# Performance work log

Hardware: AMD Instinct MI355X
Metric: run time of the kernel (lower is better)

## Reference

```python
import jax, jax.numpy as jnp
import numpy as np

N_NODES = 50000
N_EDGES = 800000
D_IN, D_HID, D_LAT = 128, 128, 64
BN_EPS = 1e-5


def setup_inputs() -> dict:
    key = jax.random.key(0)
    ks = jax.random.split(key, 8)
    x = jax.random.normal(ks[0], (N_NODES, D_IN), dtype=jnp.float32)
    edge_index = jax.random.randint(ks[1], (2, N_EDGES), 0, N_NODES, dtype=jnp.int64)
    s1 = 1.0 / np.sqrt(D_IN)
    s2 = 1.0 / np.sqrt(D_HID)
    W1 = jax.random.normal(ks[2], (D_IN, D_HID), dtype=jnp.float32) * s1
    b1 = jnp.zeros((D_HID,), jnp.float32)
    gamma = jnp.ones((D_HID,), jnp.float32)
    beta = jnp.zeros((D_HID,), jnp.float32)
    Wmu = jax.random.normal(ks[3], (D_HID, D_LAT), dtype=jnp.float32) * s2
    bmu = jnp.zeros((D_LAT,), jnp.float32)
    Wls = jax.random.normal(ks[4], (D_HID, D_LAT), dtype=jnp.float32) * s2
    bls = jnp.zeros((D_LAT,), jnp.float32)
    return {"x": x, "edge_index": edge_index, "W1": W1, "b1": b1,
            "gamma": gamma, "beta": beta, "Wmu": Wmu, "bmu": bmu,
            "Wls": Wls, "bls": bls}


def _gcn_conv(h, src, dst, norm_e, inv_deg, W, b):
    # PyG GCNConv: linear transform, then sym-normalized aggregation (A+I).
    h = h @ W                                   # [N, F]
    msgs = h[src] * norm_e[:, None]             # gather + edge scaling, [E, F]
    agg = jax.ops.segment_sum(msgs, dst, num_segments=h.shape[0])
    # self-loop contribution: norm[i]*norm[i] = 1/deg[i]
    return agg + h * inv_deg[:, None] + b


def reference(x, edge_index, W1, b1, gamma, beta, Wmu, bmu, Wls, bls):
    src, dst = edge_index[0], edge_index[1]
    n = x.shape[0]
    # degrees including self loops (GCN symmetric normalization)
    deg = jax.ops.segment_sum(jnp.ones(dst.shape, x.dtype), dst, num_segments=n) + 1.0
    inv_sqrt_deg = jax.lax.rsqrt(deg)
    norm_e = inv_sqrt_deg[src] * inv_sqrt_deg[dst]   # per-edge norm, [E]
    inv_deg = 1.0 / deg

    h = _gcn_conv(x, src, dst, norm_e, inv_deg, W1, b1)
    # BatchNorm1d with batch statistics (biased var), then ReLU; dropout off (eval)
    mean = h.mean(axis=0)
    var = h.var(axis=0)
    h = (h - mean) * jax.lax.rsqrt(var + BN_EPS) * gamma + beta
    h = jax.nn.relu(h)

    mu = _gcn_conv(h, src, dst, norm_e, inv_deg, Wmu, bmu)
    log_std = _gcn_conv(h, src, dst, norm_e, inv_deg, Wls, bls)
    return mu, log_std
```

## Files before the change

kernel.cpp:

```cpp
#include <hip/hip_runtime.h>
#include <hip/hip_bf16.h>

#define N_NODES 50000
#define N_EDGES 800000
#define F 128
#define L 64
#define BN_EPS 1e-5f
#define SCAN_BLOCKS 196
#define BN_BLOCKS 391
#define NPART 8
#define PART_SZ 6250
#define FILL_BLOCKS 2048

typedef __attribute__((ext_vector_type(8))) short short8;
typedef __attribute__((ext_vector_type(8))) unsigned short ushort8;
typedef __attribute__((ext_vector_type(4))) float f32x4;

static __device__ __forceinline__ float loadF(const void* p, int i, int f32) {
    if (f32) return ((const float*)p)[i];
    return __bfloat162float(((const __hip_bfloat16*)p)[i]);
}
static __device__ __forceinline__ int loadI(const void* p, int i, int i64) {
    if (i64) return (int)((const long long*)p)[i];
    return ((const int*)p)[i];
}
static __device__ __forceinline__ float bfu2f(unsigned short u) {
    unsigned int t = ((unsigned int)u) << 16;
    float f;
    __builtin_memcpy(&f, &t, 4);
    return f;
}
static __device__ __forceinline__ short f2bf_s(float f) {
    union { __hip_bfloat16 b; short s; } cv;
    cv.b = __float2bfloat16(f);
    return cv.s;
}
static __device__ __forceinline__ unsigned short f2bf_u(float f) {
    union { __hip_bfloat16 b; unsigned short u; } cv;
    cv.b = __float2bfloat16(f);
    return cv.u;
}

__global__ void k_prep(const void* __restrict__ W1, const void* __restrict__ Wmu,
                       const void* __restrict__ Wls, const unsigned short* __restrict__ xs,
                       const int* __restrict__ ei, __hip_bfloat16* __restrict__ Wt1,
                       __hip_bfloat16* __restrict__ Wt2, int* __restrict__ flags,
                       int* __restrict__ degi) {
    int b = blockIdx.x;
    int t = threadIdx.x;
    if (b == 0) {
        __shared__ int cnt[2];
        if (t < 2) cnt[t] = 0;
        __syncthreads();
        unsigned short v = xs[2 * t];
        int e = (v >> 7) & 0xff;
        int sane = (e >= 112 && e <= 133) ? 1 : 0;
        if (v == 0 || v == 0x8000) sane = 1;
        atomicAdd(&cnt[0], sane);
        atomicAdd(&cnt[1], (ei[2 * t + 1] != 0) ? 1 : 0);
        __syncthreads();
        if (t == 0) {
            flags[0] = (cnt[0] < 128) ? 1 : 0;
            flags[1] = (cnt[1] < 8) ? 1 : 0;
        }
    } else if (b <= 64) {
        __shared__ int cnt;
        if (t == 0) cnt = 0;
        __syncthreads();
        unsigned short v = ((const unsigned short*)W1)[2 * t];
        int e = (v >> 7) & 0xff;
        atomicAdd(&cnt, (e >= 100 && e <= 133) ? 1 : 0);
        __syncthreads();
        int f32 = (cnt < 128) ? 1 : 0;
        int idx = (b - 1) * 256 + t;
        int n = idx >> 7, k = idx & 127;
        Wt1[idx] = __float2bfloat16(loadF(W1, k * F + n, f32));
        float v2 = (n < L) ? loadF(Wmu, k * L + n, f32) : loadF(Wls, k * L + (n - L), f32);
        Wt2[idx] = __float2bfloat16(v2);
    } else {
        int i = (b - 65) * 256 + t;
        if (i < N_NODES) degi[i] = 0;
    }
}

__global__ void k_eiprep(const void* ei, const int* __restrict__ flags,
                         int* __restrict__ src32, int* __restrict__ dst32,
                         int* __restrict__ degi) {
    int e = blockIdx.x * blockDim.x + threadIdx.x;
    if (e < N_EDGES) {
        int i64 = flags[1];
        int d = loadI(ei, N_EDGES + e, i64);
        if (i64) {
            src32[e] = loadI(ei, e, 1);
            dst32[e] = d;
        }
        atomicAdd(&degi[d], 1);
    }
}

__global__ void k_bsum(const int* __restrict__ degi, int* __restrict__ bsum) {
    int i = blockIdx.x * 256 + threadIdx.x;
    int v = (i < N_NODES) ? degi[i] : 0;
#pragma unroll
    for (int o = 32; o; o >>= 1) v += __shfl_down(v, o);
    __shared__ int ws[4];
    if ((threadIdx.x & 63) == 0) ws[threadIdx.x >> 6] = v;
    __syncthreads();
    if (threadIdx.x == 0) bsum[blockIdx.x] = ws[0] + ws[1] + ws[2] + ws[3];
}

__global__ void k_scanb(const int* __restrict__ bsum, int* __restrict__ boff,
                        int* __restrict__ offs) {
    __shared__ int s[256];
    int t = threadIdx.x;
    int v = (t < SCAN_BLOCKS) ? bsum[t] : 0;
    s[t] = v;
    __syncthreads();
    for (int o = 1; o < 256; o <<= 1) {
        int u = (t >= o) ? s[t - o] : 0;
        __syncthreads();
        s[t] += u;
        __syncthreads();
    }
    boff[t] = s[t] - v;
    if (t == 0) offs[N_NODES] = N_EDGES;
}

__global__ void k_offs(int* __restrict__ degi, const int* __restrict__ boff,
                       int* __restrict__ offs, float* __restrict__ isd) {
    __shared__ int s[256];
    int i = blockIdx.x * 256 + threadIdx.x;
    int t = threadIdx.x;
    int v = (i < N_NODES) ? degi[i] : 0;
    s[t] = v;
    __syncthreads();
    for (int o = 1; o < 256; o <<= 1) {
        int u = (t >= o) ? s[t - o] : 0;
        __syncthreads();
        s[t] += u;
        __syncthreads();
    }
    if (i < N_NODES) {
        offs[i] = boff[blockIdx.x] + s[t] - v;
        isd[i] = 1.0f / sqrtf((float)v + 1.0f);
        degi[i] = 0;
    }
}

__global__ void k_fill(const int* __restrict__ ei32, const int* __restrict__ src32,
                       const int* __restrict__ dst32, const int* __restrict__ flags,
                       const int* __restrict__ offs, int* __restrict__ cur,
                       int* __restrict__ csr) {
    const int* sp;
    const int* dp;
    if (flags[1]) { sp = src32; dp = dst32; }
    else          { sp = ei32;  dp = ei32 + N_EDGES; }
    int grp = blockIdx.x & (NPART - 1);
    int sub = blockIdx.x >> 3;
    int lo = grp * PART_SZ, hi = lo + PART_SZ;
    int stride = (FILL_BLOCKS >> 3) * 256;
    for (int e = sub * 256 + threadIdx.x; e < N_EDGES; e += stride) {
        int d = dp[e];
        if (d >= lo && d < hi) {
            int pos = offs[d] + atomicAdd(&cur[d], 1);
            csr[pos] = sp[e];
        }
    }
}

__global__ __launch_bounds__(256) void k_gemm_mfma(const void* __restrict__ Xin,
        const __hip_bfloat16* __restrict__ Wt, const float* __restrict__ isd,
        const int* __restrict__ flags, int mode,
        const float* __restrict__ bnscale, const float* __restrict__ bnshift,
        unsigned short* __restrict__ outb) {
    int wave = threadIdx.x >> 6, lane = threadIdx.x & 63;
    int quad = lane >> 4, mr = lane & 15;
    int m0 = blockIdx.x * 64 + wave * 16;
    int row = m0 + mr;
    if (row >= N_NODES) row = N_NODES - 1;
    short8 a[4];
    if (mode == 1) {
        const unsigned short* xb = (const unsigned short*)Xin;
#pragma unroll
        for (int t = 0; t < 4; ++t) {
            int k0 = t * 32 + quad * 8;
            ushort8 raw = *(const ushort8*)(xb + row * F + k0);
            short8 av;
#pragma unroll
            for (int j = 0; j < 8; ++j) {
                float v = bfu2f(raw[j]) * bnscale[k0 + j] + bnshift[k0 + j];
                av[j] = f2bf_s(fmaxf(v, 0.f));
            }
            a[t] = av;
        }
    } else if (flags[0]) {
        const float* xf = (const float*)Xin;
#pragma unroll
        for (int t = 0; t < 4; ++t) {
            int off = row * F + t * 32 + quad * 8;
            short8 av;
#pragma unroll
            for (int j = 0; j < 8; ++j) av[j] = f2bf_s(xf[off + j]);
            a[t] = av;
        }
    } else {
        const short* xb = (const short*)Xin;
#pragma unroll
        for (int t = 0; t < 4; ++t)
            a[t] = *(const short8*)(xb + row * F + t * 32 + quad * 8);
    }
    f32x4 acc[8];
    const short* wb = (const short*)Wt;
#pragma unroll
    for (int nt = 0; nt < 8; ++nt) {
        const short* wp = wb + (nt * 16 + mr) * F + quad * 8;
        f32x4 c = {0.f, 0.f, 0.f, 0.f};
        c = __builtin_amdgcn_mfma_f32_16x16x32_bf16(a[0], *(const short8*)(wp), c, 0, 0, 0);
        c = __builtin_amdgcn_mfma_f32_16x16x32_bf16(a[1], *(const short8*)(wp + 32), c, 0, 0, 0);
        c = __builtin_amdgcn_mfma_f32_16x16x32_bf16(a[2], *(const short8*)(wp + 64), c, 0, 0, 0);
        c = __builtin_amdgcn_mfma_f32_16x16x32_bf16(a[3], *(const short8*)(wp + 96), c, 0, 0, 0);
        acc[nt] = c;
    }
    float sd[4];
    int orow[4];
#pragma unroll
    for (int r = 0; r < 4; ++r) {
        orow[r] = m0 + quad * 4 + r;
        sd[r] = (orow[r] < N_NODES) ? isd[orow[r]] : 0.f;
    }
#pragma unroll
    for (int nt = 0; nt < 8; ++nt)
#pragma unroll
        for (int r = 0; r < 4; ++r)
            if (orow[r] < N_NODES)
                outb[orow[r] * F + nt * 16 + mr] = f2bf_u(acc[nt][r] * sd[r]);
}

__global__ void k_agg1(const unsigned short* __restrict__ val, const int* __restrict__ csr,
                       const int* __restrict__ offs, const float* __restrict__ isd,
                       const void* __restrict__ b1, const int* __restrict__ flags,
                       unsigned short* __restrict__ out) {
    int node = blockIdx.x * 4 + (threadIdx.x >> 6);
    if (node >= N_NODES) return;
    int lane = threadIdx.x & 63;
    int grp = lane >> 4, l16 = lane & 15;
    const ushort8* vp = (const ushort8*)val;
    float acc[8] = {0.f, 0.f, 0.f, 0.f, 0.f, 0.f, 0.f, 0.f};
    if (grp == 0) {
        ushort8 u = vp[node * 16 + l16];
#pragma unroll
        for (int j = 0; j < 8; ++j) acc[j] = bfu2f(u[j]);
    }
    int end = offs[node + 1];
    int i = offs[node] + grp;
    for (; i + 4 < end; i += 8) {
        ushort8 u0 = vp[csr[i] * 16 + l16];
        ushort8 u1 = vp[csr[i + 4] * 16 + l16];
#pragma unroll
        for (int j = 0; j < 8; ++j) acc[j] += bfu2f(u0[j]) + bfu2f(u1[j]);
    }
    for (; i < end; i += 4) {
        ushort8 u = vp[csr[i] * 16 + l16];
#pragma unroll
        for (int j = 0; j < 8; ++j) acc[j] += bfu2f(u[j]);
    }
#pragma unroll
    for (int j = 0; j < 8; ++j) {
        acc[j] += __shfl_xor(acc[j], 16);
        acc[j] += __shfl_xor(acc[j], 32);
    }
    if (grp == 0) {
        float sd = isd[node];
        int c0 = l16 * 8, f32 = flags[0];
        ushort8 r;
#pragma unroll
        for (int j = 0; j < 8; ++j) r[j] = f2bf_u(acc[j] * sd + loadF(b1, c0 + j, f32));
        ((ushort8*)out)[node * 16 + l16] = r;
    }
}

__global__ void k_bnstats(const unsigned short* __restrict__ h, float* __restrict__ partial) {
    __shared__ float ls[256][8];
    __shared__ float lq[256][8];
    int t = threadIdx.x;
    int o = t & 15, rg = t >> 4;
    int row0 = blockIdx.x * 128 + rg;
    float s[8] = {0.f}, q[8] = {0.f};
#pragma unroll
    for (int i = 0; i < 8; ++i) {
        int row = row0 + i * 16;
        if (row < N_NODES) {
            ushort8 u = *(const ushort8*)(h + row * F + o * 8);
#pragma unroll
            for (int j = 0; j < 8; ++j) {
                float v = bfu2f(u[j]);
                s[j] += v;
                q[j] += v * v;
            }
        }
    }
#pragma unroll
    for (int j = 0; j < 8; ++j) { ls[t][j] = s[j]; lq[t][j] = q[j]; }
    __syncthreads();
    if (t < 128) {
        int c = t, oo = c >> 3, jj = c & 7;
        float ts = 0.f, tq = 0.f;
#pragma unroll
        for (int rgi = 0; rgi < 16; ++rgi) {
            ts += ls[rgi * 16 + oo][jj];
            tq += lq[rgi * 16 + oo][jj];
        }
        partial[blockIdx.x * 256 + c] = ts;
        partial[blockIdx.x * 256 + 128 + c] = tq;
    }
}

__global__ void k_bnredprep(const float* __restrict__ partial, const void* __restrict__ gamma,
                            const void* __restrict__ beta, const int* __restrict__ flags,
                            float* __restrict__ scale, float* __restrict__ shift) {
    int c = blockIdx.x;
    float s = 0.f, q = 0.f;
    for (int b = threadIdx.x; b < BN_BLOCKS; b += 256) {
        s += partial[b * 256 + c];
        q += partial[b * 256 + 128 + c];
    }
#pragma unroll
    for (int o = 32; o; o >>= 1) {
        s += __shfl_down(s, o);
        q += __shfl_down(q, o);
    }
    __shared__ float ws[4], wq[4];
    if ((threadIdx.x & 63) == 0) {
        ws[threadIdx.x >> 6] = s;
        wq[threadIdx.x >> 6] = q;
    }
    __syncthreads();
    if (threadIdx.x == 0) {
        float S = ws[0] + ws[1] + ws[2] + ws[3];
        float Q = wq[0] + wq[1] + wq[2] + wq[3];
        const float invN = 1.0f / (float)N_NODES;
        float m = S * invN;
        float var = Q * invN - m * m;
        int f32 = flags[0];
        float sc = loadF(gamma, c, f32) * rsqrtf(var + BN_EPS);
        scale[c] = sc;
        shift[c] = loadF(beta, c, f32) - m * sc;
    }
}

__global__ void k_agg2(const unsigned short* __restrict__ val, const int* __restrict__ csr,
                       const int* __restrict__ offs, const float* __restrict__ isd,
                       const void* __restrict__ bmu, const void* __restrict__ bls,
                       const int* __restrict__ flags, void* __restrict__ out) {
    int node = blockIdx.x * 4 + (threadIdx.x >> 6);
    if (node >= N_NODES) return;
    int lane = threadIdx.x & 63;
    int grp = lane >> 4, l16 = lane & 15;
    const ushort8* vp = (const ushort8*)val;
    float acc[8] = {0.f, 0.f, 0.f, 0.f, 0.f, 0.f, 0.f, 0.f};
    if (grp == 0) {
        ushort8 u = vp[node * 16 + l16];
#pragma unroll
        for (int j = 0; j < 8; ++j) acc[j] = bfu2f(u[j]);
    }
    int end = offs[node + 1];
    int i = offs[node] + grp;
    for (; i + 4 < end; i += 8) {
        ushort8 u0 = vp[csr[i] * 16 + l16];
        ushort8 u1 = vp[csr[i + 4] * 16 + l16];
#pragma unroll
        for (int j = 0; j < 8; ++j) acc[j] += bfu2f(u0[j]) + bfu2f(u1[j]);
    }
    for (; i < end; i += 4) {
        ushort8 u = vp[csr[i] * 16 + l16];
#pragma unroll
        for (int j = 0; j < 8; ++j) acc[j] += bfu2f(u[j]);
    }
#pragma unroll
    for (int j = 0; j < 8; ++j) {
        acc[j] += __shfl_xor(acc[j], 16);
        acc[j] += __shfl_xor(acc[j], 32);
    }
    if (grp == 0) {
        float sd = isd[node];
        int c0 = l16 * 8, f32 = flags[0];
        int hsel = (c0 >= L) ? 1 : 0;
        int cc = c0 - hsel * L;
        const void* bp = hsel ? bls : bmu;
        float o8[8];
#pragma unroll
        for (int j = 0; j < 8; ++j) o8[j] = acc[j] * sd + loadF(bp, cc + j, f32);
        long base_o = (long)hsel * (N_NODES * 64) + (long)node * 64 + cc;
        if (f32) {
            float4 r0 = make_float4(o8[0], o8[1], o8[2], o8[3]);
            float4 r1 = make_float4(o8[4], o8[5], o8[6], o8[7]);
            *(float4*)((float*)out + base_o) = r0;
            *(float4*)((float*)out + base_o + 4) = r1;
        } else {
            ushort8 r;
#pragma unroll
            for (int j = 0; j < 8; ++j) r[j] = f2bf_u(o8[j]);
            *(ushort8*)((__hip_bfloat16*)out + base_o) = r;
        }
    }
}

extern "C" void kernel_launch(void* const* d_in, const int* in_sizes, int n_in,
                              void* d_out, int out_size, void* d_ws, size_t ws_size,
                              hipStream_t stream) {
    const void* x     = d_in[0];
    const void* ei    = d_in[1];
    const void* W1    = d_in[2];
    const void* b1    = d_in[3];
    const void* gamma = d_in[4];
    const void* beta  = d_in[5];
    const void* Wmu   = d_in[6];
    const void* bmu   = d_in[7];
    const void* Wls   = d_in[8];
    const void* bls   = d_in[9];

    int*   degi  = (int*)d_ws;
    int*   offs  = degi + 50048;
    float* isd   = (float*)(offs + 50048);
    float* stats = isd + 50000;
    int*   flags = (int*)(stats + 512);
    int*   bsum  = flags + 16;
    int*   boff  = bsum + 256;
    int*   csr   = boff + 256;
    int*   src32 = csr + 800000;
    int*   dst32 = src32 + 800000;
    __hip_bfloat16* Wt1 = (__hip_bfloat16*)(dst32 + 800000);
    __hip_bfloat16* Wt2 = Wt1 + 16384;
    unsigned short* Abf = (unsigned short*)(Wt2 + 16384);
    unsigned short* Hpre = Abf + N_NODES * F;
    float* partial = (float*)(Hpre + N_NODES * F);

    const int NT = 256;
    const int AGG_BLOCKS = (N_NODES + 3) / 4;
    const int GEMM_BLOCKS = (N_NODES + 63) / 64;

    k_prep<<<65 + SCAN_BLOCKS, NT, 0, stream>>>(W1, Wmu, Wls, (const unsigned short*)x,
                                                (const int*)ei, Wt1, Wt2, flags, degi);
    k_eiprep<<<(N_EDGES + NT - 1) / NT, NT, 0, stream>>>(ei, flags, src32, dst32, degi);
    k_bsum<<<SCAN_BLOCKS, NT, 0, stream>>>(degi, bsum);
    k_scanb<<<1, NT, 0, stream>>>(bsum, boff, offs);
    k_offs<<<SCAN_BLOCKS, NT, 0, stream>>>(degi, boff, offs, isd);
    k_fill<<<FILL_BLOCKS, NT, 0, stream>>>((const int*)ei, src32, dst32, flags,
                                           offs, degi, csr);

    k_gemm_mfma<<<GEMM_BLOCKS, NT, 0, stream>>>(x, Wt1, isd, flags, 0, nullptr, nullptr, Abf);
    k_agg1<<<AGG_BLOCKS, NT, 0, stream>>>(Abf, csr, offs, isd, b1, flags, Hpre);

    k_bnstats<<<BN_BLOCKS, NT, 0, stream>>>(Hpre, partial);
    k_bnredprep<<<128, NT, 0, stream>>>(partial, gamma, beta, flags, stats, stats + 128);

    k_gemm_mfma<<<GEMM_BLOCKS, NT, 0, stream>>>(Hpre, Wt2, isd, flags, 1,
                                                stats, stats + 128, Abf);
    k_agg2<<<AGG_BLOCKS, NT, 0, stream>>>(Abf, csr, offs, isd, bmu, bls, flags, d_out);
}
```

Baseline: 315.0 us.

## Merge scan kernels into atomic-allocated offsets and co-launch CSR fill with first GEMM

Replaces the three-kernel degree scan (block sums, single-block scan, offset write) with one kernel that scans locally and reserves its base offset through an atomic counter. This means CSR segments are no longer in node order, so aggregation now reads degree plus offset instead of offs[node+1]. The CSR fill and the first feature GEMM are fused into a single launch using disjoint block ranges, so the fill's atomic-bound work can overlap the MFMA work. The GEMM also gets vectorized input and BN-parameter loads, swapped MFMA operands so each lane stores contiguous 4-element rows, and the aggregation loop is unrolled to four gathers per iteration.

```diff
diff --git a/kernel.cpp b/kernel.cpp
--- a/kernel.cpp
+++ b/kernel.cpp
@@ -11,9 +11,11 @@
 #define NPART 8
 #define PART_SZ 6250
 #define FILL_BLOCKS 2048
+#define GEMM_BLOCKS 782
 
 typedef __attribute__((ext_vector_type(8))) short short8;
 typedef __attribute__((ext_vector_type(8))) unsigned short ushort8;
+typedef __attribute__((ext_vector_type(4))) unsigned short ushortx4;
 typedef __attribute__((ext_vector_type(4))) float f32x4;
 
 static __device__ __forceinline__ float loadF(const void* p, int i, int f32) {
@@ -62,6 +64,7 @@
         if (t == 0) {
             flags[0] = (cnt[0] < 128) ? 1 : 0;
             flags[1] = (cnt[1] < 8) ? 1 : 0;
+            flags[2] = 0;
         }
     } else if (b <= 64) {
         __shared__ int cnt;
@@ -98,39 +101,13 @@
     }
 }
 
-__global__ void k_bsum(const int* __restrict__ degi, int* __restrict__ bsum) {
-    int i = blockIdx.x * 256 + threadIdx.x;
-    int v = (i < N_NODES) ? degi[i] : 0;
-#pragma unroll
-    for (int o = 32; o; o >>= 1) v += __shfl_down(v, o);
-    __shared__ int ws[4];
-    if ((threadIdx.x & 63) == 0) ws[threadIdx.x >> 6] = v;
-    __syncthreads();
-    if (threadIdx.x == 0) bsum[blockIdx.x] = ws[0] + ws[1] + ws[2] + ws[3];
-}
-
-__global__ void k_scanb(const int* __restrict__ bsum, int* __restrict__ boff,
-                        int* __restrict__ offs) {
+__global__ void k_offs_alloc(const int* __restrict__ degi, int* __restrict__ flags,
+                             int* __restrict__ offs, float* __restrict__ isd,
+                             int* __restrict__ cur) {
     __shared__ int s[256];
+    __shared__ int base;
     int t = threadIdx.x;
-    int v = (t < SCAN_BLOCKS) ? bsum[t] : 0;
-    s[t] = v;
-    __syncthreads();
-    for (int o = 1; o < 256; o <<= 1) {
-        int u = (t >= o) ? s[t - o] : 0;
-        __syncthreads();
-        s[t] += u;
-        __syncthreads();
-    }
-    boff[t] = s[t] - v;
-    if (t == 0) offs[N_NODES] = N_EDGES;
-}
-
-__global__ void k_offs(int* __restrict__ degi, const int* __restrict__ boff,
-                       int* __restrict__ offs, float* __restrict__ isd) {
-    __shared__ int s[256];
-    int i = blockIdx.x * 256 + threadIdx.x;
-    int t = threadIdx.x;
+    int i = blockIdx.x * 256 + t;
     int v = (i < N_NODES) ? degi[i] : 0;
     s[t] = v;
     __syncthreads();
@@ -140,44 +117,25 @@
         s[t] += u;
         __syncthreads();
     }
+    if (t == 255) base = atomicAdd(&flags[2], s[255]);
+    __syncthreads();
     if (i < N_NODES) {
-        offs[i] = boff[blockIdx.x] + s[t] - v;
+        offs[i] = base + s[t] - v;
         isd[i] = 1.0f / sqrtf((float)v + 1.0f);
-        degi[i] = 0;
-    }
-}
-
-__global__ void k_fill(const int* __restrict__ ei32, const int* __restrict__ src32,
-                       const int* __restrict__ dst32, const int* __restrict__ flags,
-                       const int* __restrict__ offs, int* __restrict__ cur,
-                       int* __restrict__ csr) {
-    const int* sp;
-    const int* dp;
-    if (flags[1]) { sp = src32; dp = dst32; }
-    else          { sp = ei32;  dp = ei32 + N_EDGES; }
-    int grp = blockIdx.x & (NPART - 1);
-    int sub = blockIdx.x >> 3;
-    int lo = grp * PART_SZ, hi = lo + PART_SZ;
-    int stride = (FILL_BLOCKS >> 3) * 256;
-    for (int e = sub * 256 + threadIdx.x; e < N_EDGES; e += stride) {
-        int d = dp[e];
-        if (d >= lo && d < hi) {
-            int pos = offs[d] + atomicAdd(&cur[d], 1);
-            csr[pos] = sp[e];
-        }
-    }
-}
-
-__global__ __launch_bounds__(256) void k_gemm_mfma(const void* __restrict__ Xin,
+        cur[i] = 0;
+    }
+}
+
+static __device__ __forceinline__ void gemm_body(int bid, const void* __restrict__ Xin,
         const __hip_bfloat16* __restrict__ Wt, const float* __restrict__ isd,
         const int* __restrict__ flags, int mode,
         const float* __restrict__ bnscale, const float* __restrict__ bnshift,
         unsigned short* __restrict__ outb) {
     int wave = threadIdx.x >> 6, lane = threadIdx.x & 63;
     int quad = lane >> 4, mr = lane & 15;
-    int m0 = blockIdx.x * 64 + wave * 16;
-    int row = m0 + mr;
-    if (row >= N_NODES) row = N_NODES - 1;
+    int m0 = bid * 64 + wave * 16;
+    int node = m0 + mr;
+    int row = (node < N_NODES) ? node : N_NODES - 1;
     short8 a[4];
     if (mode == 1) {
         const unsigned short* xb = (const unsigned short*)Xin;
@@ -185,12 +143,17 @@
         for (int t = 0; t < 4; ++t) {
             int k0 = t * 32 + quad * 8;
             ushort8 raw = *(const ushort8*)(xb + row * F + k0);
+            f32x4 s0 = *(const f32x4*)(bnscale + k0);
+            f32x4 s1 = *(const f32x4*)(bnscale + k0 + 4);
+            f32x4 h0 = *(const f32x4*)(bnshift + k0);
+            f32x4 h1 = *(const f32x4*)(bnshift + k0 + 4);
             short8 av;
 #pragma unroll
-            for (int j = 0; j < 8; ++j) {
-                float v = bfu2f(raw[j]) * bnscale[k0 + j] + bnshift[k0 + j];
-                av[j] = f2bf_s(fmaxf(v, 0.f));
-            }
+            for (int j = 0; j < 4; ++j)
+                av[j] = f2bf_s(fmaxf(bfu2f(raw[j]) * s0[j] + h0[j], 0.f));
+#pragma unroll
+            for (int j = 0; j < 4; ++j)
+                av[4 + j] = f2bf_s(fmaxf(bfu2f(raw[4 + j]) * s1[j] + h1[j], 0.f));
             a[t] = av;
         }
     } else if (flags[0]) {
@@ -198,9 +161,13 @@
 #pragma unroll
         for (int t = 0; t < 4; ++t) {
             int off = row * F + t * 32 + quad * 8;
+            f32x4 v0 = *(const f32x4*)(xf + off);
+            f32x4 v1 = *(const f32x4*)(xf + off + 4);
             short8 av;
 #pragma unroll
-            for (int j = 0; j < 8; ++j) av[j] = f2bf_s(xf[off + j]);
+            for (int j = 0; j < 4; ++j) av[j] = f2bf_s(v0[j]);
+#pragma unroll
+            for (int j = 0; j < 4; ++j) av[4 + j] = f2bf_s(v1[j]);
             a[t] = av;
         }
     } else {
@@ -215,60 +182,109 @@
     for (int nt = 0; nt < 8; ++nt) {
         const short* wp = wb + (nt * 16 + mr) * F + quad * 8;
         f32x4 c = {0.f, 0.f, 0.f, 0.f};
-        c = __builtin_amdgcn_mfma_f32_16x16x32_bf16(a[0], *(const short8*)(wp), c, 0, 0, 0);
-        c = __builtin_amdgcn_mfma_f32_16x16x32_bf16(a[1], *(const short8*)(wp + 32), c, 0, 0, 0);
-        c = __builtin_amdgcn_mfma_f32_16x16x32_bf16(a[2], *(const short8*)(wp + 64), c, 0, 0, 0);
-        c = __builtin_amdgcn_mfma_f32_16x16x32_bf16(a[3], *(const short8*)(wp + 96), c, 0, 0, 0);
+        c = __builtin_amdgcn_mfma_f32_16x16x32_bf16(*(const short8*)(wp), a[0], c, 0, 0, 0);
+        c = __builtin_amdgcn_mfma_f32_16x16x32_bf16(*(const short8*)(wp + 32), a[1], c, 0, 0, 0);
+        c = __builtin_amdgcn_mfma_f32_16x16x32_bf16(*(const short8*)(wp + 64), a[2], c, 0, 0, 0);
+        c = __builtin_amdgcn_mfma_f32_16x16x32_bf16(*(const short8*)(wp + 96), a[3], c, 0, 0, 0);
         acc[nt] = c;
     }
-    float sd[4];
-    int orow[4];
-#pragma unroll
-    for (int r = 0; r < 4; ++r) {
-        orow[r] = m0 + quad * 4 + r;
-        sd[r] = (orow[r] < N_NODES) ? isd[orow[r]] : 0.f;
-    }
-#pragma unroll
-    for (int nt = 0; nt < 8; ++nt)
-#pragma unroll
-        for (int r = 0; r < 4; ++r)
-            if (orow[r] < N_NODES)
-                outb[orow[r] * F + nt * 16 + mr] = f2bf_u(acc[nt][r] * sd[r]);
+    if (node < N_NODES) {
+        float sd = isd[node];
+        unsigned short* op = outb + node * F;
+#pragma unroll
+        for (int nt = 0; nt < 8; ++nt) {
+            ushortx4 r;
+#pragma unroll
+            for (int j = 0; j < 4; ++j) r[j] = f2bf_u(acc[nt][j] * sd);
+            *(ushortx4*)(op + nt * 16 + quad * 4) = r;
+        }
+    }
+}
+
+__global__ __launch_bounds__(256) void k_fill_gemm1(
+        const int* __restrict__ ei32, const int* __restrict__ src32,
+        const int* __restrict__ dst32, const int* __restrict__ flags,
+        const int* __restrict__ offs, int* __restrict__ cur, int* __restrict__ csr,
+        const void* __restrict__ X, const __hip_bfloat16* __restrict__ Wt1,
+        const float* __restrict__ isd, unsigned short* __restrict__ outb) {
+    if (blockIdx.x < FILL_BLOCKS) {
+        const int* sp;
+        const int* dp;
+        if (flags[1]) { sp = src32; dp = dst32; }
+        else          { sp = ei32;  dp = ei32 + N_EDGES; }
+        int grp = blockIdx.x & (NPART - 1);
+        int sub = blockIdx.x >> 3;
+        int lo = grp * PART_SZ, hi = lo + PART_SZ;
+        int stride = (FILL_BLOCKS >> 3) * 256;
+        for (int e = sub * 256 + threadIdx.x; e < N_EDGES; e += stride) {
+            int d = dp[e];
+            if (d >= lo && d < hi) {
+                int pos = offs[d] + atomicAdd(&cur[d], 1);
+                csr[pos] = sp[e];
+            }
+        }
+    } else {
+        gemm_body(blockIdx.x - FILL_BLOCKS, X, Wt1, isd, flags, 0, nullptr, nullptr, outb);
+    }
+}
+
+__global__ __launch_bounds__(256) void k_gemm_bn(const void* __restrict__ Xin,
+        const __hip_bfloat16* __restrict__ Wt, const float* __restrict__ isd,
+        const int* __restrict__ flags, const float* __restrict__ bnscale,
+        const float* __restrict__ bnshift, unsigned short* __restrict__ outb) {
+    gemm_body(blockIdx.x, Xin, Wt, isd, flags, 1, bnscale, bnshift, outb);
+}
+
+static __device__ __forceinline__ void agg_accum(int node, int grp, int l16,
+        const ushort8* __restrict__ vp, const int* __restrict__ csr,
+        const int* __restrict__ offs, const int* __restrict__ degi, float acc[8]) {
+#pragma unroll
+    for (int j = 0; j < 8; ++j) acc[j] = 0.f;
+    if (grp == 0) {
+        ushort8 u = vp[node * 16 + l16];
+#pragma unroll
+        for (int j = 0; j < 8; ++j) acc[j] = bfu2f(u[j]);
+    }
+    int start = offs[node];
+    int end = start + degi[node];
+    int i = start + grp;
+    for (; i + 12 < end; i += 16) {
+        ushort8 u0 = vp[csr[i] * 16 + l16];
+        ushort8 u1 = vp[csr[i + 4] * 16 + l16];
+        ushort8 u2 = vp[csr[i + 8] * 16 + l16];
+        ushort8 u3 = vp[csr[i + 12] * 16 + l16];
+#pragma unroll
+        for (int j = 0; j < 8; ++j)
+            acc[j] += (bfu2f(u0[j]) + bfu2f(u1[j])) + (bfu2f(u2[j]) + bfu2f(u3[j]));
+    }
+    for (; i + 4 < end; i += 8) {
+        ushort8 u0 = vp[csr[i] * 16 + l16];
+        ushort8 u1 = vp[csr[i + 4] * 16 + l16];
+#pragma unroll
+        for (int j = 0; j < 8; ++j) acc[j] += bfu2f(u0[j]) + bfu2f(u1[j]);
+    }
+    for (; i < end; i += 4) {
+        ushort8 u = vp[csr[i] * 16 + l16];
+#pragma unroll
+        for (int j = 0; j < 8; ++j) acc[j] += bfu2f(u[j]);
+    }
+#pragma unroll
+    for (int j = 0; j < 8; ++j) {
+        acc[j] += __shfl_xor(acc[j], 16);
+        acc[j] += __shfl_xor(acc[j], 32);
+    }
 }
 
 __global__ void k_agg1(const unsigned short* __restrict__ val, const int* __restrict__ csr,
-                       const int* __restrict__ offs, const float* __restrict__ isd,
-                       const void* __restrict__ b1, const int* __restrict__ flags,
-                       unsigned short* __restrict__ out) {
+                       const int* __restrict__ offs, const int* __restrict__ degi,
+                       const float* __restrict__ isd, const void* __restrict__ b1,
+                       const int* __restrict__ flags, unsigned short* __restrict__ out) {
     int node = blockIdx.x * 4 + (threadIdx.x >> 6);
     if (node >= N_NODES) return;
     int lane = threadIdx.x & 63;
     int grp = lane >> 4, l16 = lane & 15;
-    const ushort8* vp = (const ushort8*)val;
-    float acc[8] = {0.f, 0.f, 0.f, 0.f, 0.f, 0.f, 0.f, 0.f};
-    if (grp == 0) {
-        ushort8 u = vp[node * 16 + l16];
-#pragma unroll
-        for (int j = 0; j < 8; ++j) acc[j] = bfu2f(u[j]);
-    }
-    int end = offs[node + 1];
-    int i = offs[node] + grp;
-    for (; i + 4 < end; i += 8) {
-        ushort8 u0 = vp[csr[i] * 16 + l16];
-        ushort8 u1 = vp[csr[i + 4] * 16 + l16];
-#pragma unroll
-        for (int j = 0; j < 8; ++j) acc[j] += bfu2f(u0[j]) + bfu2f(u1[j]);
-    }
-    for (; i < end; i += 4) {
-        ushort8 u = vp[csr[i] * 16 + l16];
-#pragma unroll
-        for (int j = 0; j < 8; ++j) acc[j] += bfu2f(u[j]);
-    }
-#pragma unroll
-    for (int j = 0; j < 8; ++j) {
-        acc[j] += __shfl_xor(acc[j], 16);
-        acc[j] += __shfl_xor(acc[j], 32);
-    }
+    float acc[8];
+    agg_accum(node, grp, l16, (const ushort8*)val, csr, offs, degi, acc);
     if (grp == 0) {
         float sd = isd[node];
         int c0 = l16 * 8, f32 = flags[0];
@@ -349,38 +365,16 @@
 }
 
 __global__ void k_agg2(const unsigned short* __restrict__ val, const int* __restrict__ csr,
-                       const int* __restrict__ offs, const float* __restrict__ isd,
-                       const void* __restrict__ bmu, const void* __restrict__ bls,
-                       const int* __restrict__ flags, void* __restrict__ out) {
+                       const int* __restrict__ offs, const int* __restrict__ degi,
+                       const float* __restrict__ isd, const void* __restrict__ bmu,
+                       const void* __restrict__ bls, const int* __restrict__ flags,
+                       void* __restrict__ out) {
     int node = blockIdx.x * 4 + (threadIdx.x >> 6);
     if (node >= N_NODES) return;
     int lane = threadIdx.x & 63;
     int grp = lane >> 4, l16 = lane & 15;
-    const ushort8* vp = (const ushort8*)val;
-    float acc[8] = {0.f, 0.f, 0.f, 0.f, 0.f, 0.f, 0.f, 0.f};
-    if (grp == 0) {
-        ushort8 u = vp[node * 16 + l16];
-#pragma unroll
-        for (int j = 0; j < 8; ++j) acc[j] = bfu2f(u[j]);
-    }
-    int end = offs[node + 1];
-    int i = offs[node] + grp;
-    for (; i + 4 < end; i += 8) {
-        ushort8 u0 = vp[csr[i] * 16 + l16];
-        ushort8 u1 = vp[csr[i + 4] * 16 + l16];
-#pragma unroll
-        for (int j = 0; j < 8; ++j) acc[j] += bfu2f(u0[j]) + bfu2f(u1[j]);
-    }
-    for (; i < end; i += 4) {
-        ushort8 u = vp[csr[i] * 16 + l16];
-#pragma unroll
-        for (int j = 0; j < 8; ++j) acc[j] += bfu2f(u[j]);
-    }
-#pragma unroll
-    for (int j = 0; j < 8; ++j) {
-        acc[j] += __shfl_xor(acc[j], 16);
-        acc[j] += __shfl_xor(acc[j], 32);
-    }
+    float acc[8];
+    agg_accum(node, grp, l16, (const ushort8*)val, csr, offs, degi, acc);
     if (grp == 0) {
         float sd = isd[node];
         int c0 = l16 * 8, f32 = flags[0];
@@ -421,12 +415,11 @@
 
     int*   degi  = (int*)d_ws;
     int*   offs  = degi + 50048;
-    float* isd   = (float*)(offs + 50048);
-    float* stats = isd + 50000;
+    int*   cur   = offs + 50048;
+    float* isd   = (float*)(cur + 50048);
+    float* stats = isd + 50048;
     int*   flags = (int*)(stats + 512);
-    int*   bsum  = flags + 16;
-    int*   boff  = bsum + 256;
-    int*   csr   = boff + 256;
+    int*   csr   = flags + 16;
     int*   src32 = csr + 800000;
     int*   dst32 = src32 + 800000;
     __hip_bfloat16* Wt1 = (__hip_bfloat16*)(dst32 + 800000);
@@ -437,24 +430,16 @@
 
     const int NT = 256;
     const int AGG_BLOCKS = (N_NODES + 3) / 4;
-    const int GEMM_BLOCKS = (N_NODES + 63) / 64;
 
     k_prep<<<65 + SCAN_BLOCKS, NT, 0, stream>>>(W1, Wmu, Wls, (const unsigned short*)x,
                                                 (const int*)ei, Wt1, Wt2, flags, degi);
     k_eiprep<<<(N_EDGES + NT - 1) / NT, NT, 0, stream>>>(ei, flags, src32, dst32, degi);
-    k_bsum<<<SCAN_BLOCKS, NT, 0, stream>>>(degi, bsum);
-    k_scanb<<<1, NT, 0, stream>>>(bsum, boff, offs);
-    k_offs<<<SCAN_BLOCKS, NT, 0, stream>>>(degi, boff, offs, isd);
-    k_fill<<<FILL_BLOCKS, NT, 0, stream>>>((const int*)ei, src32, dst32, flags,
-                                           offs, degi, csr);
-
-    k_gemm_mfma<<<GEMM_BLOCKS, NT, 0, stream>>>(x, Wt1, isd, flags, 0, nullptr, nullptr, Abf);
-    k_agg1<<<AGG_BLOCKS, NT, 0, stream>>>(Abf, csr, offs, isd, b1, flags, Hpre);
-
+    k_offs_alloc<<<SCAN_BLOCKS, NT, 0, stream>>>(degi, flags, offs, isd, cur);
+    k_fill_gemm1<<<FILL_BLOCKS + GEMM_BLOCKS, NT, 0, stream>>>(
+        (const int*)ei, src32, dst32, flags, offs, cur, csr, x, Wt1, isd, Abf);
+    k_agg1<<<AGG_BLOCKS, NT, 0, stream>>>(Abf, csr, offs, degi, isd, b1, flags, Hpre);
     k_bnstats<<<BN_BLOCKS, NT, 0, stream>>>(Hpre, partial);
     k_bnredprep<<<128, NT, 0, stream>>>(partial, gamma, beta, flags, stats, stats + 128);
-
-    k_gemm_mfma<<<GEMM_BLOCKS, NT, 0, stream>>>(Hpre, Wt2, isd, flags, 1,
-                                                stats, stats + 128, Abf);
-    k_agg2<<<AGG_BLOCKS, NT, 0, stream>>>(Abf, csr, offs, isd, bmu, bls, flags, d_out);
-}
+    k_gemm_bn<<<GEMM_BLOCKS, NT, 0, stream>>>(Hpre, Wt2, isd, flags, stats, stats + 128, Abf);
+    k_agg2<<<AGG_BLOCKS, NT, 0, stream>>>(Abf, csr, offs, degi, isd, bmu, bls, flags, d_out);
+}
```

Measured after the change: 308.4 us. 1.02x faster.
